# Optimization experiments

Hardware: AMD Instinct MI355X
Metric: run time of the kernel (lower is better)

The kernel has to match this reference:

```python
import jax, jax.numpy as jnp
import numpy as np


def _rel_index(h):
    # static relative-position index for an h x h grid (torch meshgrid 'ij')
    coords = np.stack(np.meshgrid(np.arange(h), np.arange(h), indexing='ij'))  # (2,h,h)
    cf = coords.reshape(2, -1)                       # (2, N)
    rel = cf[:, :, None] - cf[:, None, :]            # (2, N, N)
    rel = rel.transpose(1, 2, 0)                     # (N, N, 2)
    rel[..., 0] += h - 1
    rel[..., 1] += h - 1
    rel[..., 0] *= 2 * h - 1
    return rel.sum(-1)                               # (N, N) int


def _conv2d_s2(x, w, b):
    y = jax.lax.conv_general_dilated(x, w, window_strides=(2, 2),
                                     padding=[(1, 1), (1, 1)],
                                     dimension_numbers=('NCHW', 'OIHW', 'NCHW'))
    return y + b[None, :, None, None]


def _attn(z, qkv_w, qkv_b, out_w, out_b, table, heads):
    # H == reduce_size for every layer in this config, so no interp of K/V.
    B, C, H, W = z.shape
    N = H * W
    inner = qkv_w.shape[0] // 3
    d = inner // heads
    qkv = jnp.einsum('oc,bchw->bohw', qkv_w, z) + qkv_b[None, :, None, None]
    q, k, v = jnp.split(qkv, 3, axis=1)
    # channel layout is (dim_head, heads) with heads fastest (einops '(dim_head heads)')
    def split_heads(t):
        return t.reshape(B, d, heads, N).transpose(0, 2, 3, 1)  # b h n d
    q, k, v = split_heads(q), split_heads(k), split_heads(v)
    att = jnp.einsum('bhid,bhjd->bhij', q, k)
    idx = _rel_index(H)
    bias = table[idx.reshape(-1)].reshape(N, N, heads).transpose(2, 0, 1)  # (h, N, N)
    att = (att + bias[None]) * (d ** -0.5)  # bias added BEFORE scale, as in source
    att = jax.nn.softmax(att, axis=-1)
    o = jnp.einsum('bhij,bhjd->bhid', att, v)
    o = o.transpose(0, 3, 1, 2).reshape(B, d * heads, H, W)  # back to (dim_head heads) layout
    return jnp.einsum('oc,bchw->bohw', out_w, o) + out_b[None, :, None, None]


def setup_inputs() -> dict:
    key = jax.random.key(0)
    ks = jax.random.split(key, 24)
    heads = 3
    dims = [16, 32, 64]
    in_chs = [1, 16, 32]
    reds = [32, 16, 8]
    inp = {'x': jax.random.normal(ks[0], (32, 1, 64, 64), dtype=jnp.float32)}
    j = 1
    for i, (dim, cin, r) in enumerate(zip(dims, in_chs, reds), start=1):
        dh = dim // heads
        inner = dh * heads
        inp[f'conv{i}_w'] = jax.random.normal(ks[j], (dim, cin, 3, 3), dtype=jnp.float32) * 0.05; j += 1
        inp[f'conv{i}_b'] = jax.random.normal(ks[j], (dim,), dtype=jnp.float32) * 0.01; j += 1
        inp[f'qkv{i}_w'] = jax.random.normal(ks[j], (inner * 3, dim), dtype=jnp.float32) * 0.05; j += 1
        inp[f'qkv{i}_b'] = jax.random.normal(ks[j], (inner * 3,), dtype=jnp.float32) * 0.01; j += 1
        inp[f'out{i}_w'] = jax.random.normal(ks[j], (dim, inner), dtype=jnp.float32) * 0.05; j += 1
        inp[f'out{i}_b'] = jax.random.normal(ks[j], (dim,), dtype=jnp.float32) * 0.01; j += 1
        inp[f'rel{i}'] = jax.random.normal(ks[j], ((2 * r - 1) * (2 * r - 1), heads), dtype=jnp.float32) * 0.02; j += 1
    inp['cls_w'] = jax.random.normal(ks[j], (10, 64), dtype=jnp.float32) * 0.05; j += 1
    inp['cls_b'] = jax.random.normal(ks[j], (10,), dtype=jnp.float32) * 0.01
    return inp


def reference(x, conv1_w, conv1_b, qkv1_w, qkv1_b, out1_w, out1_b, rel1,
              conv2_w, conv2_b, qkv2_w, qkv2_b, out2_w, out2_b, rel2,
              conv3_w, conv3_b, qkv3_w, qkv3_b, out3_w, out3_b, rel3,
              cls_w, cls_b):
    heads = 3
    z = jax.nn.relu(_conv2d_s2(x, conv1_w, conv1_b))
    z = _attn(z, qkv1_w, qkv1_b, out1_w, out1_b, rel1, heads) + z
    z = jax.nn.relu(_conv2d_s2(z, conv2_w, conv2_b))
    z = _attn(z, qkv2_w, qkv2_b, out2_w, out2_b, rel2, heads) + z
    z = jax.nn.relu(_conv2d_s2(z, conv3_w, conv3_b))
    z = _attn(z, qkv3_w, qkv3_b, out3_w, out3_b, rel3, heads) + z
    z = z.mean(axis=(2, 3))           # adaptive avg pool to 1x1 + flatten -> (B, 64)
    cls_output = z @ cls_w.T + cls_b  # CLS_head linear (dropout inactive in eval)
    return (z, cls_output)
```

## Files before the change

### kernel.cpp

```cpp
#include <hip/hip_runtime.h>
#include <math.h>

#define CDIV(a, b) (((a) + (b) - 1) / (b))

#define LOG2E 1.4426950408889634f
#define SC5  (0.44721359549996f * LOG2E)
#define SC10 (0.31622776601684f * LOG2E)
#define SC21 (0.21821789023599f * LOG2E)
#define EXP2(x) __builtin_amdgcn_exp2f(x)

template <int N> __device__ inline void waitcnt_vm() {
    if constexpr (N == 0) asm volatile("s_waitcnt vmcnt(0)" ::: "memory");
    else if constexpr (N == 3) asm volatile("s_waitcnt vmcnt(3)" ::: "memory");
    else static_assert(N < 0, "unsupported vmcnt literal");
}

template <int CIN, int HIN, int COUT, int HOUT, int INNER, int DP, int KVRS, int KVD, int TPX,
          int BS>
__global__ void __launch_bounds__(BS) conv_qkv(const float* __restrict__ in,
                                               const float* __restrict__ cw,
                                               const float* __restrict__ cb,
                                               const float* __restrict__ qw,
                                               const float* __restrict__ qb,
                                               float* __restrict__ z, float* __restrict__ q,
                                               float* __restrict__ kv) {
    constexpr int N = HOUT * HOUT;
    constexpr int ZSTR = COUT + 4;
    __shared__ float zt[TPX * ZSTR];
    const int b  = blockIdx.x / (N / TPX);
    const int n0 = (blockIdx.x % (N / TPX)) * TPX;
    const int tid = threadIdx.x;

    for (int idx = tid; idx < COUT * TPX; idx += BS) {
        int c = idx / TPX, px = idx % TPX;
        int n = n0 + px;
        int ho = n / HOUT, wo = n % HOUT;
        float a0 = cb[c], a1 = 0.f, a2 = 0.f;
        for (int ci = 0; ci < CIN; ++ci) {
            const float* ip = in + (size_t)(b * CIN + ci) * HIN * HIN;
            const float* wp = cw + (size_t)(c * CIN + ci) * 9;
            #pragma unroll
            for (int kh = 0; kh < 3; ++kh) {
                int hi = 2 * ho + kh - 1;
                if (hi < 0 || hi >= HIN) continue;
                float av = 0.f;
                #pragma unroll
                for (int kw = 0; kw < 3; ++kw) {
                    int wi = 2 * wo + kw - 1;
                    if (wi < 0 || wi >= HIN) continue;
                    av = fmaf(wp[kh * 3 + kw], ip[hi * HIN + wi], av);
                }
                if (kh == 0) a0 += av; else if (kh == 1) a1 += av; else a2 += av;
            }
        }
        float acc = fmaxf((a0 + a1) + a2, 0.f);
        zt[px * ZSTR + c] = acc;
        z[((size_t)(b * COUT) + c) * N + n] = acc;
    }
    __syncthreads();

    constexpr int OC3 = 3 * INNER;
    constexpr int NF4 = COUT / 4;
    for (int idx = tid; idx < OC3 * TPX; idx += BS) {
        int oc = idx / TPX, px = idx % TPX;
        const float4* wp4 = (const float4*)(qw + (size_t)oc * COUT);
        const float4* z4  = (const float4*)(zt + px * ZSTR);
        float vs[4] = {0.f, 0.f, 0.f, 0.f};
        #pragma unroll
        for (int c4 = 0; c4 < NF4; ++c4) {
            float4 a = wp4[c4], bb = z4[c4];
            float& v = vs[c4 & 3];
            v = fmaf(a.x, bb.x, v); v = fmaf(a.y, bb.y, v);
            v = fmaf(a.z, bb.z, v); v = fmaf(a.w, bb.w, v);
        }
        float val = qb[oc] + ((vs[0] + vs[1]) + (vs[2] + vs[3]));
        int part = oc / INNER;
        int r = oc - part * INNER;
        int hh = r % 3, dd = r / 3;
        size_t n = n0 + px;
        if (part == 0)
            q[((size_t)(b * 3 + hh) * N + n) * DP + dd] = val;
        else
            kv[((size_t)(b * 3 + hh) * N + n) * KVRS + (part - 1) * KVD + dd] = val;
    }
}

template <int CPREV, int INNERP, int DPREV, int HINW, int COUT, int HOUT, int INNER, int DP,
          int KVRS, int KVD, int TPX, int BS>
__global__ void __launch_bounds__(BS) fused_oc(const float* __restrict__ o1,
                                               const float* __restrict__ ow,
                                               const float* __restrict__ ob,
                                               const float* __restrict__ zres,
                                               const float* __restrict__ cw,
                                               const float* __restrict__ cb,
                                               const float* __restrict__ qw,
                                               const float* __restrict__ qb,
                                               float* __restrict__ z, float* __restrict__ q,
                                               float* __restrict__ kv) {
    constexpr int N2 = HOUT * HOUT;
    constexpr int N1 = HINW * HINW;
    constexpr int TROWS = TPX / HOUT;
    constexpr int HR = 2 * TROWS + 1;
    constexpr int HALO = HR * HINW;
    constexpr int ZSTR = COUT + 4;
    __shared__ float smem[INNERP * HALO + CPREV * HALO];
    float* o1s = smem;
    float* zh  = smem + INNERP * HALO;
    float* zt  = smem;
    static_assert(TPX * ZSTR <= INNERP * HALO, "zt overlay fits");
    const int b  = blockIdx.x / (N2 / TPX);
    const int n0 = (blockIdx.x % (N2 / TPX)) * TPX;
    const int tid = threadIdx.x;
    const int ho0 = n0 / HOUT;
    const int row0 = 2 * ho0 - 1;

    for (int t = tid; t < INNERP * HALO; t += BS) {
        int hd = t / HALO, p = t - hd * HALO;
        int row = row0 + p / HINW;
        float v = 0.f;
        if (row >= 0 && row < HINW)
            v = o1[((size_t)(b * INNERP + hd)) * N1 + row * HINW + (p % HINW)];
        o1s[t] = v;
    }
    __syncthreads();

    for (int t = tid; t < CPREV * HALO; t += BS) {
        int ci = t / HALO, p = t - ci * HALO;
        int row = row0 + p / HINW;
        float val = 0.f;
        if (row >= 0 && row < HINW) {
            int n1 = row * HINW + (p % HINW);
            const float* wp = ow + (size_t)ci * INNERP;
            float v0 = 0.f, v1 = 0.f, v2 = 0.f;
            for (int dd = 0; dd < DPREV; ++dd) {
                v0 = fmaf(wp[dd * 3 + 0], o1s[(0 * DPREV + dd) * HALO + p], v0);
                v1 = fmaf(wp[dd * 3 + 1], o1s[(1 * DPREV + dd) * HALO + p], v1);
                v2 = fmaf(wp[dd * 3 + 2], o1s[(2 * DPREV + dd) * HALO + p], v2);
            }
            val = ob[ci] + zres[((size_t)(b * CPREV) + ci) * N1 + n1] + (v0 + v1) + v2;
        }
        zh[t] = val;
    }
    __syncthreads();

    for (int idx = tid; idx < COUT * TPX; idx += BS) {
        int c = idx / TPX, px = idx - (idx / TPX) * TPX;
        int hol = px / HOUT, wo = px - hol * HOUT;
        float a0 = cb[c], a1 = 0.f, a2 = 0.f;
        for (int ci = 0; ci < CPREV; ++ci) {
            const float* zp = zh + ci * HALO + (2 * hol) * HINW;
            const float* wp = cw + (size_t)(c * CPREV + ci) * 9;
            #pragma unroll
            for (int kw = 0; kw < 3; ++kw) {
                int col = 2 * wo + kw - 1;
                if (col < 0 || col >= HINW) continue;
                a0 = fmaf(wp[0 * 3 + kw], zp[0 * HINW + col], a0);
                a1 = fmaf(wp[1 * 3 + kw], zp[1 * HINW + col], a1);
                a2 = fmaf(wp[2 * 3 + kw], zp[2 * HINW + col], a2);
            }
        }
        float acc = fmaxf((a0 + a1) + a2, 0.f);
        zt[px * ZSTR + c] = acc;
        z[((size_t)(b * COUT) + c) * N2 + n0 + px] = acc;
    }
    __syncthreads();

    constexpr int OC3 = 3 * INNER;
    constexpr int NF4 = COUT / 4;
    for (int idx = tid; idx < OC3 * TPX; idx += BS) {
        int oc = idx / TPX, px = idx % TPX;
        const float4* wp4 = (const float4*)(qw + (size_t)oc * COUT);
        const float4* z4  = (const float4*)(zt + px * ZSTR);
        float vs[4] = {0.f, 0.f, 0.f, 0.f};
        #pragma unroll
        for (int c4 = 0; c4 < NF4; ++c4) {
            float4 a = wp4[c4], bb = z4[c4];
            float& v = vs[c4 & 3];
            v = fmaf(a.x, bb.x, v); v = fmaf(a.y, bb.y, v);
            v = fmaf(a.z, bb.z, v); v = fmaf(a.w, bb.w, v);
        }
        float val = qb[oc] + ((vs[0] + vs[1]) + (vs[2] + vs[3]));
        int part = oc / INNER;
        int r = oc - part * INNER;
        int hh = r % 3, dd = r / 3;
        size_t n = n0 + px;
        if (part == 0)
            q[((size_t)(b * 3 + hh) * N2 + n) * DP + dd] = val;
        else
            kv[((size_t)(b * 3 + hh) * N2 + n) * KVRS + (part - 1) * KVD + dd] = val;
    }
}

template <int D, int QP, int RS, int RPT, int TILE, int NW>
__global__ void __launch_bounds__(NW * 64) attn_big(const float* __restrict__ q,
                                                    const float* __restrict__ kv,
                                                    const float* __restrict__ table,
                                                    float* __restrict__ o, int N, int log2Hg,
                                                    int T, float scale2) {
    extern __shared__ float smem[];
    float* tb = smem;
    float* comb = smem;
    constexpr int BT = NW * 64;
    constexpr int ROWS = 64 * RPT;
    constexpr int CSTR = (D % 2 == 0) ? (D + 3) : (D + 2);
    constexpr int TBYTES = TILE * RS * 4;
    constexpr int LPT = CDIV(TBYTES, 1024);
    constexpr bool FULLT = (TBYTES % 1024) == 0;
    static_assert(LPT == 3, "vmcnt literal below assumes 3 loads per tile");

    const int bh = blockIdx.x % 96;
    const int chunk = blockIdx.x / 96;
    const int h = bh % 3;
    const int tid = threadIdx.x;
    const int wave = tid >> 6;
    const int lane = tid & 63;
    const int Hg = 1 << log2Hg;
    const int W2 = 2 * Hg - 1;
    const int base = chunk * ROWS;

    float* kvw = smem + ((T + 3) & ~3) + wave * (2 * TILE * RS);

    for (int t = tid; t < T; t += BT) tb[t] = table[t * 3 + h] * scale2;

    float qr[RPT][D];
    const float* tbp[RPT];
    #pragma unroll
    for (int r = 0; r < RPT; ++r) {
        int i = base + lane + 64 * r;
        const float* qg = q + ((size_t)bh * N + i) * QP;
        #pragma unroll
        for (int dd = 0; dd < D; ++dd) qr[r][dd] = qg[dd];
        tbp[r] = tb + (((i >> log2Hg) + Hg - 1) * W2 + (i & (Hg - 1)) + Hg - 1);
    }

    float acc[RPT][D];
    float lsum[RPT];
    #pragma unroll
    for (int r = 0; r < RPT; ++r) {
        lsum[r] = 0.f;
        #pragma unroll
        for (int dd = 0; dd < D; ++dd) acc[r][dd] = 0.f;
    }

    const float* kvbase = kv + (size_t)bh * N * RS;
    const int NJ = N / NW;
    const int NT = NJ / TILE;
    const int j0 = wave * NJ;

    auto stage = [&](int bufIdx, int t) {
        const float* srcf = kvbase + (size_t)(j0 + t * TILE) * RS;
        float* dstf = kvw + bufIdx * (TILE * RS);
        #pragma unroll
        for (int x = 0; x < LPT; ++x) {
            if (FULLT || (x * 1024 + lane * 16) < TBYTES) {
                const void* g = (const void*)(srcf + x * 256 + lane * 4);
                void* l = (void*)(dstf + x * 256);
                __builtin_amdgcn_global_load_lds(
                    (const __attribute__((address_space(1))) void*)g,
                    (__attribute__((address_space(3))) void*)l, 16, 0, 0);
            }
        }
    };

    stage(0, 0);
    if (NT > 1) stage(1, 1);

    __syncthreads();

    for (int t = 0; t < NT; ++t) {
        const float* curb = kvw + (t & 1) * (TILE * RS);
        const int jt = j0 + t * TILE;
        for (int jg = 0; jg < TILE; jg += 4) {
            #pragma unroll
            for (int k = 0; k < 4; ++k) {
                const int j = jt + jg + k;
                const float* kr = curb + (jg + k) * RS;
                const int joff = (j >> log2Hg) * W2 + (j & (Hg - 1));
                #pragma unroll
                for (int r = 0; r < RPT; ++r) {
                    float s = 0.f;
                    #pragma unroll
                    for (int dd = 0; dd < D; ++dd) s = fmaf(qr[r][dd], kr[dd], s);
                    float e = EXP2(fmaf(s, scale2, tbp[r][-joff]));
                    lsum[r] += e;
                    #pragma unroll
                    for (int dd = 0; dd < D; ++dd) acc[r][dd] = fmaf(e, kr[D + dd], acc[r][dd]);
                }
            }
        }
        if (t + 2 < NT) {
            asm volatile("s_waitcnt lgkmcnt(0)" ::: "memory");
            stage(t & 1, t + 2);
            waitcnt_vm<3>();
        } else if (t + 1 < NT) {
            waitcnt_vm<0>();
        }
    }

    __syncthreads();
    #pragma unroll
    for (int r = 0; r < RPT; ++r) {
        float* cp = comb + (size_t)(wave * ROWS + lane + 64 * r) * CSTR;
        #pragma unroll
        for (int dd = 0; dd < D; ++dd) cp[dd] = acc[r][dd];
        cp[D] = lsum[r];
    }
    __syncthreads();
    if (tid < ROWS) {
        float af[D];
        #pragma unroll
        for (int dd = 0; dd < D; ++dd) af[dd] = 0.f;
        float lf = 0.f;
        #pragma unroll
        for (int wv = 0; wv < NW; ++wv) {
            const float* cp = comb + (size_t)(wv * ROWS + tid) * CSTR;
            #pragma unroll
            for (int dd = 0; dd < D; ++dd) af[dd] += cp[dd];
            lf += cp[D];
        }
        float inv = 1.0f / lf;
        int i = base + tid;
        #pragma unroll
        for (int dd = 0; dd < D; ++dd)
            o[((size_t)bh * D + dd) * N + i] = af[dd] * inv;
    }
}

__global__ void __launch_bounds__(512) attn_small(const float* __restrict__ q,
                                                  const float* __restrict__ kv,
                                                  const float* __restrict__ table,
                                                  float* __restrict__ o, float scale2) {
    constexpr int D = 21, DP = 24, NN = 64;
    constexpr int CSTR = 23;
    __shared__ float smem[8 * NN * CSTR];
    float* kvs = smem;
    float* tb = kvs + NN * 2 * DP;
    float* comb = smem;

    const int bh = blockIdx.x;
    const int h = bh % 3;
    const int tid = threadIdx.x;
    const int wave = tid >> 6;
    const int lane = tid & 63;

    {
        const float4* kvg = (const float4*)(kv + (size_t)bh * NN * 2 * DP);
        float4* kvs4 = (float4*)kvs;
        for (int t = tid; t < NN * 2 * DP / 4; t += 512) kvs4[t] = kvg[t];
        for (int t = tid; t < 225; t += 512) tb[t] = table[t * 3 + h] * scale2;
    }

    const int i = lane;
    const float* qg = q + ((size_t)bh * NN + i) * DP;
    float qr[D];
    #pragma unroll
    for (int dd = 0; dd < D; ++dd) qr[dd] = qg[dd];
    const int ibase = ((i >> 3) + 7) * 15 + (i & 7) + 7;
    __syncthreads();

    float acc[D];
    #pragma unroll
    for (int dd = 0; dd < D; ++dd) acc[dd] = 0.f;
    float lsum = 0.f;

    const int j0 = wave * 8;
    #pragma unroll
    for (int jj = 0; jj < 8; ++jj) {
        const int j = j0 + jj;
        float4 r4[12];
        const float4* rp = (const float4*)(kvs + j * 2 * DP);
        #pragma unroll
        for (int x = 0; x < 12; ++x) r4[x] = rp[x];
        const float* kr = (const float*)r4;
        const float* vr = kr + DP;
        const int joff = (j >> 3) * 15 + (j & 7);
        float s = 0.f;
        #pragma unroll
        for (int dd = 0; dd < D; ++dd) s = fmaf(qr[dd], kr[dd], s);
        float e = EXP2(fmaf(s, scale2, tb[ibase - joff]));
        lsum += e;
        #pragma unroll
        for (int dd = 0; dd < D; ++dd) acc[dd] = fmaf(e, vr[dd], acc[dd]);
    }

    __syncthreads();
    {
        float* cp = comb + (size_t)(wave * NN + lane) * CSTR;
        #pragma unroll
        for (int dd = 0; dd < D; ++dd) cp[dd] = acc[dd];
        cp[D] = lsum;
    }
    __syncthreads();
    if (tid < NN) {
        float af[D];
        #pragma unroll
        for (int dd = 0; dd < D; ++dd) af[dd] = 0.f;
        float lf = 0.f;
        #pragma unroll
        for (int wv = 0; wv < 8; ++wv) {
            const float* cp = comb + (size_t)(wv * NN + tid) * CSTR;
            #pragma unroll
            for (int dd = 0; dd < D; ++dd) af[dd] += cp[dd];
            lf += cp[D];
        }
        float inv = 1.0f / lf;
        #pragma unroll
        for (int dd = 0; dd < D; ++dd)
            o[((size_t)bh * D + dd) * NN + tid] = af[dd] * inv;
    }
}

__global__ void __launch_bounds__(256) tail(const float* __restrict__ o,
                                            const float* __restrict__ ow,
                                            const float* __restrict__ ob,
                                            const float* __restrict__ zin,
                                            const float* __restrict__ cw,
                                            const float* __restrict__ cb,
                                            float* __restrict__ out) {
    __shared__ float os[63 * 64];
    __shared__ float zt[64 * 65];
    __shared__ float p[64];
    const int b = blockIdx.x;
    const int tid = threadIdx.x;
    for (int t = tid; t < 63 * 64; t += 256) os[t] = o[(size_t)(b * 63) * 64 + t];
    __syncthreads();
    for (int idx = tid; idx < 64 * 64; idx += 256) {
        int c = idx >> 6, n = idx & 63;
        const float* wp = ow + (size_t)c * 63;
        float v0 = 0.f, v1 = 0.f, v2 = 0.f;
        for (int dd = 0; dd < 21; ++dd) {
            v0 = fmaf(wp[dd * 3 + 0], os[(0  + dd) * 64 + n], v0);
            v1 = fmaf(wp[dd * 3 + 1], os[(21 + dd) * 64 + n], v1);
            v2 = fmaf(wp[dd * 3 + 2], os[(42 + dd) * 64 + n], v2);
        }
        zt[c * 65 + n] = ob[c] + zin[((size_t)(b * 64) + c) * 64 + n] + (v0 + v1) + v2;
    }
    __syncthreads();
    if (tid < 64) {
        float s = 0.f;
        #pragma unroll
        for (int n = 0; n < 64; ++n) s += zt[tid * 65 + n];
        s *= (1.0f / 64.0f);
        p[tid] = s;
        out[b * 64 + tid] = s;
    }
    __syncthreads();
    if (tid < 10) {
        float val = cb[tid];
        const float* wp = cw + (size_t)tid * 64;
        #pragma unroll
        for (int kk = 0; kk < 64; ++kk) val = fmaf(wp[kk], p[kk], val);
        out[2048 + b * 10 + tid] = val;
    }
}

extern "C" void kernel_launch(void* const* d_in, const int* in_sizes, int n_in,
                              void* d_out, int out_size, void* d_ws, size_t ws_size,
                              hipStream_t stream) {
    float* ws = (float*)d_ws;
    float* Zc1 = ws;
    float* Zc2 = Zc1 + 524288;
    float* Q   = Zc2 + 262144;
    float* KV  = Q + 786432;
    float* O   = KV + 1572864;

    float* out = (float*)d_out;

    conv_qkv<1, 64, 16, 32, 15, 8, 12, 5, 32, 512><<<32 * 32, 512, 0, stream>>>(
        (const float*)d_in[0], (const float*)d_in[1], (const float*)d_in[2],
        (const float*)d_in[3], (const float*)d_in[4], Zc1, Q, KV);
    attn_big<5, 8, 12, 2, 64, 4><<<96 * 8, 256, 40464, stream>>>(
        Q, KV, (const float*)d_in[7], O, 1024, 5, 3969, SC5);

    fused_oc<16, 15, 5, 32, 32, 16, 30, 12, 20, 10, 16, 512><<<32 * 16, 512, 0, stream>>>(
        O, (const float*)d_in[5], (const float*)d_in[6], Zc1,
        (const float*)d_in[8], (const float*)d_in[9],
        (const float*)d_in[10], (const float*)d_in[11], Zc2, Q, KV);
    attn_big<10, 12, 20, 1, 32, 8><<<96 * 4, 512, 44816, stream>>>(
        Q, KV, (const float*)d_in[14], O, 256, 4, 961, SC10);

    fused_oc<32, 30, 10, 16, 64, 8, 63, 24, 48, 24, 8, 512><<<32 * 8, 512, 0, stream>>>(
        O, (const float*)d_in[12], (const float*)d_in[13], Zc2,
        (const float*)d_in[15], (const float*)d_in[16],
        (const float*)d_in[17], (const float*)d_in[18], Zc1, Q, KV);
    attn_small<<<96, 512, 0, stream>>>(Q, KV, (const float*)d_in[21], O, SC21);

    tail<<<32, 256, 0, stream>>>(
        O, (const float*)d_in[19], (const float*)d_in[20], Zc1,
        (const float*)d_in[22], (const float*)d_in[23], out);
}
```

Baseline: 248.4 us.

## Fuse final attention with tail projection and single-buffer layer-2 attention

Merges the last-layer attention kernel with the output projection/pool/classifier tail into one kernel per batch. Each block now handles all three heads, with six waves splitting keys in halves, and the attention output stays in LDS instead of going through global memory. This removes one launch and a global round-trip, but drops to 32 blocks, so parallelism in the attention stage falls. Separately, the layer-2 attn_big gets an NBUF template parameter and runs single-buffered with a smaller LDS allocation. Since NT is one there, this is meant to raise occupancy.

```diff
diff --git a/kernel.cpp b/kernel.cpp
--- a/kernel.cpp
+++ b/kernel.cpp
@@ -191,7 +191,7 @@
     }
 }
 
-template <int D, int QP, int RS, int RPT, int TILE, int NW>
+template <int D, int QP, int RS, int RPT, int TILE, int NW, int NBUF>
 __global__ void __launch_bounds__(NW * 64) attn_big(const float* __restrict__ q,
                                                     const float* __restrict__ kv,
                                                     const float* __restrict__ table,
@@ -218,7 +218,7 @@
     const int W2 = 2 * Hg - 1;
     const int base = chunk * ROWS;
 
-    float* kvw = smem + ((T + 3) & ~3) + wave * (2 * TILE * RS);
+    float* kvw = smem + ((T + 3) & ~3) + wave * (NBUF * TILE * RS);
 
     for (int t = tid; t < T; t += BT) tb[t] = table[t * 3 + h] * scale2;
 
@@ -263,12 +263,12 @@
     };
 
     stage(0, 0);
-    if (NT > 1) stage(1, 1);
+    if (NBUF > 1 && NT > 1) stage(1, 1);
 
     __syncthreads();
 
     for (int t = 0; t < NT; ++t) {
-        const float* curb = kvw + (t & 1) * (TILE * RS);
+        const float* curb = kvw + (t & (NBUF - 1)) * (TILE * RS);
         const int jt = j0 + t * TILE;
         for (int jg = 0; jg < TILE; jg += 4) {
             #pragma unroll
@@ -288,11 +288,11 @@
                 }
             }
         }
-        if (t + 2 < NT) {
+        if (NBUF > 1 && t + 2 < NT) {
             asm volatile("s_waitcnt lgkmcnt(0)" ::: "memory");
             stage(t & 1, t + 2);
             waitcnt_vm<3>();
-        } else if (t + 1 < NT) {
+        } else if (NBUF > 1 && t + 1 < NT) {
             waitcnt_vm<0>();
         }
     }
@@ -326,35 +326,47 @@
     }
 }
 
-__global__ void __launch_bounds__(512) attn_small(const float* __restrict__ q,
-                                                  const float* __restrict__ kv,
-                                                  const float* __restrict__ table,
-                                                  float* __restrict__ o, float scale2) {
-    constexpr int D = 21, DP = 24, NN = 64;
-    constexpr int CSTR = 23;
-    __shared__ float smem[8 * NN * CSTR];
-    float* kvs = smem;
-    float* tb = kvs + NN * 2 * DP;
-    float* comb = smem;
-
-    const int bh = blockIdx.x;
-    const int h = bh % 3;
+__global__ void __launch_bounds__(512) attn_tail(const float* __restrict__ q,
+                                                 const float* __restrict__ kv,
+                                                 const float* __restrict__ table,
+                                                 const float* __restrict__ ow,
+                                                 const float* __restrict__ ob,
+                                                 const float* __restrict__ zin,
+                                                 const float* __restrict__ cw,
+                                                 const float* __restrict__ cb,
+                                                 float* __restrict__ out, float scale2) {
+    constexpr int D = 21, DP = 24, NN = 64, CSTR = 23;
+    __shared__ float smem[12864];
+    float* kvs   = smem;
+    float* tb    = smem + 9216;
+    float* comb  = smem;
+    float* o_lds = smem + 8832;
+    float* zt    = smem;
+    float* p     = smem + 4160;
+    const int b = blockIdx.x;
     const int tid = threadIdx.x;
     const int wave = tid >> 6;
     const int lane = tid & 63;
 
     {
-        const float4* kvg = (const float4*)(kv + (size_t)bh * NN * 2 * DP);
+        const float4* kvg = (const float4*)(kv + (size_t)(b * 3) * NN * 2 * DP);
         float4* kvs4 = (float4*)kvs;
-        for (int t = tid; t < NN * 2 * DP / 4; t += 512) kvs4[t] = kvg[t];
-        for (int t = tid; t < 225; t += 512) tb[t] = table[t * 3 + h] * scale2;
-    }
-
+        for (int t = tid; t < 3 * NN * 2 * DP / 4; t += 512) kvs4[t] = kvg[t];
+        for (int t = tid; t < 3 * 225; t += 512) {
+            int hh = t / 225, tt = t - hh * 225;
+            tb[t] = table[tt * 3 + hh] * scale2;
+        }
+    }
+
+    const int hh = wave >> 1;
+    const bool active = (wave < 6);
     const int i = lane;
-    const float* qg = q + ((size_t)bh * NN + i) * DP;
     float qr[D];
-    #pragma unroll
-    for (int dd = 0; dd < D; ++dd) qr[dd] = qg[dd];
+    if (active) {
+        const float* qg = q + ((size_t)(b * 3 + hh) * NN + i) * DP;
+        #pragma unroll
+        for (int dd = 0; dd < D; ++dd) qr[dd] = qg[dd];
+    }
     const int ibase = ((i >> 3) + 7) * 15 + (i & 7) + 7;
     __syncthreads();
 
@@ -362,76 +374,58 @@
     #pragma unroll
     for (int dd = 0; dd < D; ++dd) acc[dd] = 0.f;
     float lsum = 0.f;
-
-    const int j0 = wave * 8;
-    #pragma unroll
-    for (int jj = 0; jj < 8; ++jj) {
-        const int j = j0 + jj;
-        float4 r4[12];
-        const float4* rp = (const float4*)(kvs + j * 2 * DP);
-        #pragma unroll
-        for (int x = 0; x < 12; ++x) r4[x] = rp[x];
-        const float* kr = (const float*)r4;
-        const float* vr = kr + DP;
-        const int joff = (j >> 3) * 15 + (j & 7);
-        float s = 0.f;
-        #pragma unroll
-        for (int dd = 0; dd < D; ++dd) s = fmaf(qr[dd], kr[dd], s);
-        float e = EXP2(fmaf(s, scale2, tb[ibase - joff]));
-        lsum += e;
-        #pragma unroll
-        for (int dd = 0; dd < D; ++dd) acc[dd] = fmaf(e, vr[dd], acc[dd]);
-    }
-
-    __syncthreads();
-    {
+    if (active) {
+        const float* tbh = tb + hh * 225;
+        const float* kvh = kvs + hh * (NN * 2 * DP);
+        const int j0 = (wave & 1) * 32;
+        #pragma unroll 4
+        for (int jj = 0; jj < 32; ++jj) {
+            const int j = j0 + jj;
+            float4 r4[12];
+            const float4* rp = (const float4*)(kvh + j * 2 * DP);
+            #pragma unroll
+            for (int x = 0; x < 12; ++x) r4[x] = rp[x];
+            const float* kr = (const float*)r4;
+            const float* vr = kr + DP;
+            const int joff = (j >> 3) * 15 + (j & 7);
+            float s = 0.f;
+            #pragma unroll
+            for (int dd = 0; dd < D; ++dd) s = fmaf(qr[dd], kr[dd], s);
+            float e = EXP2(fmaf(s, scale2, tbh[ibase - joff]));
+            lsum += e;
+            #pragma unroll
+            for (int dd = 0; dd < D; ++dd) acc[dd] = fmaf(e, vr[dd], acc[dd]);
+        }
+    }
+    __syncthreads();
+
+    if (active) {
         float* cp = comb + (size_t)(wave * NN + lane) * CSTR;
         #pragma unroll
         for (int dd = 0; dd < D; ++dd) cp[dd] = acc[dd];
         cp[D] = lsum;
     }
     __syncthreads();
-    if (tid < NN) {
-        float af[D];
-        #pragma unroll
-        for (int dd = 0; dd < D; ++dd) af[dd] = 0.f;
-        float lf = 0.f;
-        #pragma unroll
-        for (int wv = 0; wv < 8; ++wv) {
-            const float* cp = comb + (size_t)(wv * NN + tid) * CSTR;
-            #pragma unroll
-            for (int dd = 0; dd < D; ++dd) af[dd] += cp[dd];
-            lf += cp[D];
-        }
-        float inv = 1.0f / lf;
+
+    if (tid < 192) {
+        int h2 = tid >> 6, ii = tid & 63;
+        const float* c0 = comb + (size_t)((h2 * 2 + 0) * NN + ii) * CSTR;
+        const float* c1 = comb + (size_t)((h2 * 2 + 1) * NN + ii) * CSTR;
+        float inv = 1.0f / (c0[D] + c1[D]);
         #pragma unroll
         for (int dd = 0; dd < D; ++dd)
-            o[((size_t)bh * D + dd) * NN + tid] = af[dd] * inv;
-    }
-}
-
-__global__ void __launch_bounds__(256) tail(const float* __restrict__ o,
-                                            const float* __restrict__ ow,
-                                            const float* __restrict__ ob,
-                                            const float* __restrict__ zin,
-                                            const float* __restrict__ cw,
-                                            const float* __restrict__ cb,
-                                            float* __restrict__ out) {
-    __shared__ float os[63 * 64];
-    __shared__ float zt[64 * 65];
-    __shared__ float p[64];
-    const int b = blockIdx.x;
-    const int tid = threadIdx.x;
-    for (int t = tid; t < 63 * 64; t += 256) os[t] = o[(size_t)(b * 63) * 64 + t];
-    __syncthreads();
-    for (int idx = tid; idx < 64 * 64; idx += 256) {
+            o_lds[(h2 * 21 + dd) * 64 + ii] = (c0[dd] + c1[dd]) * inv;
+    }
+    __syncthreads();
+
+    for (int idx = tid; idx < 64 * 64; idx += 512) {
         int c = idx >> 6, n = idx & 63;
         const float* wp = ow + (size_t)c * 63;
         float v0 = 0.f, v1 = 0.f, v2 = 0.f;
         for (int dd = 0; dd < 21; ++dd) {
-            v0 = fmaf(wp[dd * 3 + 0], os[(0  + dd) * 64 + n], v0);
-            v1 = fmaf(wp[dd * 3 + 1], os[(21 + dd) * 64 + n], v1);
-            v2 = fmaf(wp[dd * 3 + 2], os[(42 + dd) * 64 + n], v2);
+            v0 = fmaf(wp[dd * 3 + 0], o_lds[(0  + dd) * 64 + n], v0);
+            v1 = fmaf(wp[dd * 3 + 1], o_lds[(21 + dd) * 64 + n], v1);
+            v2 = fmaf(wp[dd * 3 + 2], o_lds[(42 + dd) * 64 + n], v2);
         }
         zt[c * 65 + n] = ob[c] + zin[((size_t)(b * 64) + c) * 64 + n] + (v0 + v1) + v2;
     }
@@ -469,23 +463,22 @@
     conv_qkv<1, 64, 16, 32, 15, 8, 12, 5, 32, 512><<<32 * 32, 512, 0, stream>>>(
         (const float*)d_in[0], (const float*)d_in[1], (const float*)d_in[2],
         (const float*)d_in[3], (const float*)d_in[4], Zc1, Q, KV);
-    attn_big<5, 8, 12, 2, 64, 4><<<96 * 8, 256, 40464, stream>>>(
+    attn_big<5, 8, 12, 2, 64, 4, 2><<<96 * 8, 256, 40464, stream>>>(
         Q, KV, (const float*)d_in[7], O, 1024, 5, 3969, SC5);
 
     fused_oc<16, 15, 5, 32, 32, 16, 30, 12, 20, 10, 16, 512><<<32 * 16, 512, 0, stream>>>(
         O, (const float*)d_in[5], (const float*)d_in[6], Zc1,
         (const float*)d_in[8], (const float*)d_in[9],
         (const float*)d_in[10], (const float*)d_in[11], Zc2, Q, KV);
-    attn_big<10, 12, 20, 1, 32, 8><<<96 * 4, 512, 44816, stream>>>(
+    attn_big<10, 12, 20, 1, 32, 8, 1><<<96 * 4, 512, 26624, stream>>>(
         Q, KV, (const float*)d_in[14], O, 256, 4, 961, SC10);
 
     fused_oc<32, 30, 10, 16, 64, 8, 63, 24, 48, 24, 8, 512><<<32 * 8, 512, 0, stream>>>(
         O, (const float*)d_in[12], (const float*)d_in[13], Zc2,
         (const float*)d_in[15], (const float*)d_in[16],
         (const float*)d_in[17], (const float*)d_in[18], Zc1, Q, KV);
-    attn_small<<<96, 512, 0, stream>>>(Q, KV, (const float*)d_in[21], O, SC21);
-
-    tail<<<32, 256, 0, stream>>>(
-        O, (const float*)d_in[19], (const float*)d_in[20], Zc1,
-        (const float*)d_in[22], (const float*)d_in[23], out);
-}
+
+    attn_tail<<<32, 512, 0, stream>>>(
+        Q, KV, (const float*)d_in[21], (const float*)d_in[19], (const float*)d_in[20],
+        Zc1, (const float*)d_in[22], (const float*)d_in[23], out, SC21);
+}
```

New measurement: 249.4 us. About the same (+0.4%).
